# Performance work log

Measured on AMD Instinct MI355X. Metric: run time of the kernel, lower is better.

The kernel has to match this reference:

```python
import jax, jax.numpy as jnp
import numpy as np

# dims
B, A, L, P = 8, 64, 256, 20
T_HIST, SD, MF = 10, 8, 6
H, NH, NL = 256, 8, 3
C, S = 64, 30
# config scalars
DT, MAX_SPEED, MAX_ACCEL, MAX_CURV, SAFETY = 0.1, 15.0, 5.0, 0.3, 1.5
CW, BW, LAW = 1.0, 0.1, 0.5
MAX_STEP = MAX_SPEED * DT
LN_EPS = 1e-5


def _ln(x, g, b):
    m = x.mean(-1, keepdims=True)
    v = ((x - m) ** 2).mean(-1, keepdims=True)
    return (x - m) / jnp.sqrt(v + LN_EPS) * g + b


def setup_inputs() -> dict:
    key = jax.random.key(0)
    ks = jax.random.split(key, 24)
    f32 = jnp.float32
    def rn(k, shape, s=0.02):
        return jax.random.normal(k, shape, dtype=f32) * s
    return {
        'ego_history': jax.random.normal(ks[0], (B, T_HIST, SD), dtype=f32),
        'agent_states': jax.random.normal(ks[1], (B, A, SD), dtype=f32) * 5.0,
        'map_polylines': jax.random.normal(ks[2], (B, L, P, MF), dtype=f32) * 5.0,
        # encoder params (jax layout: x @ W, W is [in, out])
        'enc_ego_w': rn(ks[3], (SD, H)), 'enc_ego_b': jnp.zeros((H,), f32),
        'enc_agent_w': rn(ks[4], (SD, H)), 'enc_agent_b': jnp.zeros((H,), f32),
        'enc_map_w': rn(ks[5], (MF, H)), 'enc_map_b': jnp.zeros((H,), f32),
        'enc_ln_g': jnp.ones((H,), f32), 'enc_ln_b': jnp.zeros((H,), f32),
        # shared cross-attention (torch MHA layout: in_proj [3H,H])
        'attn_in_w': rn(ks[6], (3 * H, H)), 'attn_in_b': jnp.zeros((3 * H,), f32),
        'attn_out_w': rn(ks[7], (H, H)), 'attn_out_b': jnp.zeros((H,), f32),
        # per-layer MLPs, stacked over NL
        'mlp_w1': rn(ks[8], (NL, H, 2 * H)), 'mlp_b1': jnp.zeros((NL, 2 * H), f32),
        'mlp_w2': rn(ks[9], (NL, 2 * H, H)), 'mlp_b2': jnp.zeros((NL, H), f32),
        'pl_ln_g': jnp.ones((H,), f32), 'pl_ln_b': jnp.zeros((H,), f32),
        # heads
        'traj_w': rn(ks[10], (H, C * S * 2)), 'traj_b': jnp.zeros((C * S * 2,), f32),
        'score_w': rn(ks[11], (H, C)), 'score_b': jnp.zeros((C,), f32),
    }


def reference(ego_history, agent_states, map_polylines,
              enc_ego_w, enc_ego_b, enc_agent_w, enc_agent_b, enc_map_w, enc_map_b,
              enc_ln_g, enc_ln_b,
              attn_in_w, attn_in_b, attn_out_w, attn_out_b,
              mlp_w1, mlp_b1, mlp_w2, mlp_b2,
              pl_ln_g, pl_ln_b, traj_w, traj_b, score_w, score_b):
    # ---- vector encoder ----
    ego_tok = (ego_history[:, -1] @ enc_ego_w + enc_ego_b)[:, None, :]       # [B,1,H]
    agent_tok = agent_states @ enc_agent_w + enc_agent_b                     # [B,A,H]
    map_tok = (map_polylines @ enc_map_w + enc_map_b).mean(axis=2)           # [B,L,H]
    tokens = _ln(jnp.concatenate([ego_tok, agent_tok, map_tok], axis=1), enc_ln_g, enc_ln_b)
    lane_points = map_polylines[..., :2]                                     # [B,L,P,2]

    # ---- planner core: shared cross-attn, per-layer MLP, shared LayerNorm ----
    hd = H // NH
    wq, wk, wv = jnp.split(attn_in_w, 3, axis=0)
    bq, bk, bv = jnp.split(attn_in_b, 3)
    K = (tokens @ wk.T + bk).reshape(B, -1, NH, hd).transpose(0, 2, 1, 3)    # [B,h,N,d]
    V = (tokens @ wv.T + bv).reshape(B, -1, NH, hd).transpose(0, 2, 1, 3)
    fused = tokens[:, :1, :]                                                 # ego query [B,1,H]
    for i in range(NL):
        Q = (fused @ wq.T + bq).reshape(B, 1, NH, hd).transpose(0, 2, 1, 3)
        att = jax.nn.softmax(jnp.einsum('bhqd,bhkd->bhqk', Q, K) / (hd ** 0.5), axis=-1)
        attended = jnp.einsum('bhqk,bhkd->bhqd', att, V).transpose(0, 2, 1, 3).reshape(B, 1, H)
        attended = attended @ attn_out_w.T + attn_out_b
        h = jax.nn.gelu(fused @ mlp_w1[i] + mlp_b1[i], approximate=False)
        fused = _ln(fused + attended + (h @ mlp_w2[i] + mlp_b2[i]), pl_ln_g, pl_ln_b)
    fused = fused[:, 0, :]                                                   # [B,H]

    deltas = jnp.tanh((fused @ traj_w + traj_b).reshape(B, C, S, 2)) * MAX_STEP
    start_xy = ego_history[:, -1, :2]
    traj = start_xy[:, None, None, :] + jnp.cumsum(deltas, axis=2)           # [B,C,S,2]
    logits = fused @ score_w + score_b                                       # [B,C]
    scores = jax.nn.softmax(logits, axis=-1)

    # ---- kinematic feasibility ----
    vel = (traj[:, :, 1:] - traj[:, :, :-1]) / DT                            # [B,C,S-1,2]
    acc = (vel[:, :, 1:] - vel[:, :, :-1]) / DT
    d1 = traj[:, :, 1:] - traj[:, :, :-1]
    dd = d1[:, :, 1:] - d1[:, :, :-1]
    cross = d1[:, :, :-1, 0] * dd[..., 1] - d1[:, :, :-1, 1] * dd[..., 0]
    curv = jnp.abs(cross) / jnp.clip(jnp.linalg.norm(d1[:, :, :-1], axis=-1) ** 3, 1e-6)
    feasible = ((jnp.linalg.norm(vel, axis=-1).max(-1) <= MAX_SPEED)
                & (jnp.linalg.norm(acc, axis=-1).max(-1) <= MAX_ACCEL)
                & (curv.max(-1) <= MAX_CURV))                                # [B,C]

    # ---- collision check against agent positions ----
    cdiff = traj[:, :, :, None, :] - agent_states[:, None, None, :, :2]      # [B,C,S,A,2]
    min_distance = jnp.linalg.norm(cdiff, axis=-1).min(axis=(2, 3))          # [B,C]
    collision_free = min_distance >= SAFETY

    # ---- lane distance: pairwise min over (steps, lanes, points) ----
    t = traj.reshape(B, C * S, 2)
    lp = lane_points.reshape(B, L * P, 2)
    d2m = (jnp.sum(t * t, -1)[:, :, None] + jnp.sum(lp * lp, -1)[:, None, :]
           - 2.0 * jnp.einsum('bnx,bmx->bnm', t, lp))                        # [B,C*S,L*P]
    lane_distance = jnp.sqrt(jnp.clip(d2m, 0.0)).reshape(B, C, S * L * P).min(-1)
    lane_mask = lane_distance <= SAFETY * 3.0

    ldir = (lane_points[:, :, -1, :] - lane_points[:, :, 0, :]).mean(axis=1)
    ldir = ldir / jnp.clip(jnp.linalg.norm(ldir, axis=-1, keepdims=True), 1e-6)
    tdir = traj[:, :, -1, :] - traj[:, :, 0, :]
    tdir = tdir / jnp.clip(jnp.linalg.norm(tdir, axis=-1, keepdims=True), 1e-6)
    lane_alignment = jnp.sum(tdir * ldir[:, None, :], -1)                    # [B,C]

    # ---- masked selection ----
    valid = feasible & collision_free & lane_mask & (lane_alignment >= 0.0)
    safe_scores = jnp.where(valid, scores, -1.0)
    selected_index = jnp.where(valid.any(-1), safe_scores.argmax(-1), scores.argmax(-1))
    selected_trajectory = jnp.take_along_axis(traj, selected_index[:, None, None, None], axis=1)[:, 0]

    constraint_cost = (CW * jax.nn.relu(SAFETY - min_distance)
                       + BW * lane_distance + LAW * jax.nn.relu(1.0 - lane_alignment))
    return (traj, logits, scores, selected_index, selected_trajectory,
            min_distance, lane_distance, lane_alignment, constraint_cost)
```

## Files before the change

### kernel.cpp

```cpp
#include <hip/hip_runtime.h>
#include <math.h>
#include <stddef.h>

#define B_   8
#define A_   64
#define L_   256
#define P_   20
#define SD_  8
#define MF_  6
#define H_   256
#define NH_  8
#define HD_  32
#define NL_  3
#define C_   64
#define S_   30
#define N_   321
#define NTOK (B_*N_)

__device__ inline float waveSum(float v){
#pragma unroll
  for(int o=32;o;o>>=1) v += __shfl_down(v,o,64);
  return v;
}

__global__ void __launch_bounds__(256) k_prep_encode(
    const float* __restrict__ ego, const float* __restrict__ agents,
    const float* __restrict__ mp,
    const float* __restrict__ w_ego, const float* __restrict__ b_ego,
    const float* __restrict__ w_ag,  const float* __restrict__ b_ag,
    const float* __restrict__ w_map, const float* __restrict__ b_map,
    const float* __restrict__ ln_g,  const float* __restrict__ ln_b,
    const float* __restrict__ attn_in_w, const float* __restrict__ attn_out_w,
    float* __restrict__ tokens,
    float* __restrict__ wqT, float* __restrict__ wkT,
    float* __restrict__ wvT, float* __restrict__ aowT,
    float* __restrict__ ldir){
  int blk = blockIdx.x;
  int j = threadIdx.x;
  __shared__ float tile_s[64][65];
  __shared__ float in_s[SD_];
  __shared__ __align__(16) float arr[120];
  __shared__ float red[8];

  if(blk < NTOK){
    int b = blk / N_;
    int n = blk % N_;
    const float* W; const float* bias; int D;
    if(n==0){
      if(j<SD_) in_s[j] = ego[(b*10 + 9)*SD_ + j];
      W=w_ego; bias=b_ego; D=SD_;
    } else if(n<=A_){
      int a=n-1;
      if(j<SD_) in_s[j] = agents[(size_t)(b*A_+a)*SD_ + j];
      W=w_ag; bias=b_ag; D=SD_;
    } else {
      int l=n-1-A_;
      if(j<30) ((float4*)arr)[j] = ((const float4*)(mp + (size_t)(b*L_+l)*120))[j];
      __syncthreads();
      if(j<MF_){
        float s=0.f;
#pragma unroll
        for(int p=0;p<P_;p++) s += arr[p*MF_+j];
        in_s[j] = s * (1.0f/P_);
      }
      W=w_map; bias=b_map; D=MF_;
    }
    __syncthreads();
    float acc = bias[j];
    for(int d=0;d<D;d++) acc += in_s[d]*W[d*H_ + j];
    float s1=acc, s2=acc*acc;
#pragma unroll
    for(int o=32;o;o>>=1){ s1+=__shfl_down(s1,o,64); s2+=__shfl_down(s2,o,64); }
    if((j&63)==0){ red[j>>6]=s1; red[4+(j>>6)]=s2; }
    __syncthreads();
    float m = (red[0]+red[1]+red[2]+red[3]) * (1.0f/H_);
    float v = (red[4]+red[5]+red[6]+red[7]) * (1.0f/H_) - m*m;
    tokens[(size_t)blk*H_ + j] = (acc-m)*rsqrtf(v+1e-5f)*ln_g[j] + ln_b[j];
  } else if(blk < NTOK+64){
    int tid2 = blk - NTOK;
    int mat = tid2 >> 4;
    int tile = tid2 & 15;
    int jt = (tile>>2)*64, dt = (tile&3)*64;
    const float* src; float* dst;
    if(mat==0){ src = attn_in_w;            dst = wqT; }
    else if(mat==1){ src = attn_in_w + 256*H_; dst = wkT; }
    else if(mat==2){ src = attn_in_w + 512*H_; dst = wvT; }
    else { src = attn_out_w; dst = aowT; }
    int c = j & 63, r0 = (j>>6)*16;
#pragma unroll
    for(int r=0;r<16;r++) tile_s[r0+r][c] = src[(size_t)(jt + r0 + r)*H_ + dt + c];
    __syncthreads();
#pragma unroll
    for(int r=0;r<16;r++) dst[(size_t)(dt + r0 + r)*H_ + jt + c] = tile_s[c][r0+r];
  } else {
    int b = blk - (NTOK+64);
    const float* p0 = mp + (size_t)(b*L_ + j)*120;
    float dx = p0[19*MF_+0]-p0[0];
    float dy = p0[19*MF_+1]-p0[1];
#pragma unroll
    for(int o=32;o;o>>=1){ dx+=__shfl_down(dx,o,64); dy+=__shfl_down(dy,o,64); }
    if((j&63)==0){ red[j>>6]=dx; red[4+(j>>6)]=dy; }
    __syncthreads();
    if(j==0){
      float sx = (red[0]+red[1]+red[2]+red[3])*(1.0f/L_);
      float sy = (red[4]+red[5]+red[6]+red[7])*(1.0f/L_);
      float nm = fmaxf(sqrtf(sx*sx+sy*sy), 1e-6f);
      ldir[b*2]=sx/nm; ldir[b*2+1]=sy/nm;
    }
  }
}

__global__ void __launch_bounds__(256) k_kv(
    const float* __restrict__ tokens,
    const float* __restrict__ wkT, const float* __restrict__ wvT,
    const float* __restrict__ attn_in_b,
    float* __restrict__ K, float* __restrict__ V){
  int base = blockIdx.x * 8;
  int j = threadIdx.x;
  __shared__ float tok_s[8][H_];
#pragma unroll
  for(int t=0;t<8;t++) tok_s[t][j] = tokens[(size_t)(base+t)*H_ + j];
  __syncthreads();
  float bk = attn_in_b[256+j], bv = attn_in_b[512+j];
  float aK[8], aV[8];
#pragma unroll
  for(int t=0;t<8;t++){ aK[t]=bk; aV[t]=bv; }
#pragma unroll 4
  for(int d=0;d<H_;d++){
    float wk = wkT[d*H_+j], wv = wvT[d*H_+j];
#pragma unroll
    for(int t=0;t<8;t++){ float x=tok_s[t][d]; aK[t]+=x*wk; aV[t]+=x*wv; }
  }
#pragma unroll
  for(int t=0;t<8;t++){
    K[(size_t)(base+t)*H_+j]=aK[t];
    V[(size_t)(base+t)*H_+j]=aV[t];
  }
}

__global__ void __launch_bounds__(512) k_attn_mlp1(
    const float* __restrict__ tokens, const float* __restrict__ y_in,
    const float* __restrict__ K, const float* __restrict__ V,
    const float* __restrict__ wqT, const float* __restrict__ attn_in_b,
    const float* __restrict__ mlp_w1, const float* __restrict__ mlp_b1,
    const float* __restrict__ pl_g, const float* __restrict__ pl_b,
    float* __restrict__ fusedv, float* __restrict__ h1v,
    float* __restrict__ attv, int layer){
  const int b = blockIdx.x & 7, h = blockIdx.x >> 3;
  const int t = threadIdx.x;
  __shared__ __align__(16) float x_s[H_];
  __shared__ __align__(16) float q_s[HD_];
  __shared__ float att_s[N_+7];
  __shared__ float part1[512];
  __shared__ float part2[512];
  __shared__ float redA[8], redB[8];

  float yv = 0.f;
  if(t < H_){
    if(layer==0){
      x_s[t] = tokens[((size_t)b*N_)*H_ + t];
    } else {
      yv = y_in[b*H_ + t];
      float s1=yv, s2=yv*yv;
#pragma unroll
      for(int o=32;o;o>>=1){ s1+=__shfl_down(s1,o,64); s2+=__shfl_down(s2,o,64); }
      if((t&63)==0){ redA[t>>6]=s1; redB[t>>6]=s2; }
    }
  }
  __syncthreads();
  if(layer!=0 && t < H_){
    float m = (redA[0]+redA[1]+redA[2]+redA[3])*(1.0f/H_);
    float v = (redB[0]+redB[1]+redB[2]+redB[3])*(1.0f/H_) - m*m;
    x_s[t] = (yv-m)*rsqrtf(v+1e-5f)*pl_g[t] + pl_b[t];
  }
  __syncthreads();
  if(h==0 && t < H_) fusedv[b*H_+t] = x_s[t];

  {
    int c=t&31, ks=t>>5;
    const float* w = wqT + (size_t)(ks*16)*H_ + h*HD_ + c;
    float a=0.f;
#pragma unroll
    for(int d=0;d<16;d++) a += x_s[ks*16+d]*w[(size_t)d*H_];
    part1[t]=a;
  }
  {
    int c2=t&63, k2=t>>6;
    const float* w1 = mlp_w1 + (size_t)layer*H_*512 + (size_t)(k2*32)*512 + h*64 + c2;
    float a=0.f;
#pragma unroll
    for(int d=0;d<32;d++) a += x_s[k2*32+d]*w1[(size_t)d*512];
    part2[t]=a;
  }
  __syncthreads();
  if(t<32){
    float q = attn_in_b[h*HD_+t];
#pragma unroll
    for(int ks=0;ks<16;ks++) q += part1[ks*32+t];
    q_s[t]=q;
  }
  if(t<64){
    float v = mlp_b1[layer*512 + h*64 + t];
#pragma unroll
    for(int k2=0;k2<8;k2++) v += part2[k2*64+t];
    h1v[b*512 + h*64 + t] = v*0.5f*(1.0f+erff(v*0.70710678118654752f));
  }
  __syncthreads();

  float s0 = -3.0e38f;
  if(t < N_){
    const float4* kp=(const float4*)(K + ((size_t)(b*N_+t))*H_ + h*HD_);
    const float4* qp=(const float4*)q_s;
    float s=0.f;
#pragma unroll
    for(int i=0;i<8;i++){ float4 kk=kp[i], qq=qp[i]; s+=kk.x*qq.x+kk.y*qq.y+kk.z*qq.z+kk.w*qq.w; }
    s0 = s*0.17677669529663687f;
  }
  float mx = s0;
#pragma unroll
  for(int o=32;o;o>>=1) mx = fmaxf(mx, __shfl_xor(mx,o,64));
  if((t&63)==0) redA[t>>6]=mx;
  __syncthreads();
  mx = fmaxf(fmaxf(fmaxf(redA[0],redA[1]),fmaxf(redA[2],redA[3])),
             fmaxf(fmaxf(redA[4],redA[5]),fmaxf(redA[6],redA[7])));
  float p0 = 0.f;
  if(t < N_){ p0 = expf(s0-mx); att_s[t]=p0; }
  float lsum = p0;
#pragma unroll
  for(int o=32;o;o>>=1) lsum += __shfl_xor(lsum,o,64);
  if((t&63)==0) redB[t>>6]=lsum;
  __syncthreads();

  {
    int o=t&31, ks=t>>5;
    int n0=ks*20, n1=(ks==15)?N_:n0+20;
    const float* Vp = V + ((size_t)(b*N_))*H_ + h*HD_ + o;
    float a=0.f;
#pragma unroll 5
    for(int n=n0;n<n1;n++) a += att_s[n]*Vp[(size_t)n*H_];
    part1[t]=a;
  }
  __syncthreads();
  if(t<32){
    float inv = 1.0f/(redB[0]+redB[1]+redB[2]+redB[3]+redB[4]+redB[5]+redB[6]+redB[7]);
    float a=0.f;
#pragma unroll
    for(int ks=0;ks<16;ks++) a += part1[ks*32+t];
    attv[b*H_ + h*HD_ + t] = a*inv;
  }
}

__global__ void __launch_bounds__(512) k_out_mlp2(
    const float* __restrict__ attv, const float* __restrict__ h1v,
    const float* __restrict__ fusedv,
    const float* __restrict__ aowT, const float* __restrict__ attn_out_b,
    const float* __restrict__ mlp_w2, const float* __restrict__ mlp_b2,
    float* __restrict__ y, int layer){
  int b  = blockIdx.x >> 4;
  int cg = blockIdx.x & 15;
  int t = threadIdx.x;
  int c = t & 15, rs = t >> 4;
  int col = cg*16 + c;
  __shared__ float xa_s[H_];
  __shared__ float xh_s[512];
  __shared__ float part[16][33];
  if(t < H_) xa_s[t] = attv[b*H_ + t];
  xh_s[t] = h1v[b*512 + t];
  __syncthreads();
  float acc = 0.f;
  int r0 = rs*24, r1 = r0+24;
  int rEndA = r1 < 256 ? r1 : 256;
#pragma unroll 8
  for(int r=r0; r<rEndA; ++r) acc += xa_s[r]*aowT[(size_t)r*H_ + col];
  const float* w2 = mlp_w2 + (size_t)layer*512*H_;
  int rBegB = r0 > 256 ? r0 : 256;
#pragma unroll 8
  for(int r=rBegB; r<r1; ++r){
    int rr = r-256;
    acc += xh_s[rr]*w2[(size_t)rr*H_ + col];
  }
  part[c][rs] = acc;
  __syncthreads();
  if(t < 16){
    int colo = cg*16 + t;
    float s = 0.f;
#pragma unroll
    for(int k=0;k<32;k++) s += part[t][k];
    y[b*H_ + colo] = s + attn_out_b[colo] + mlp_b2[layer*H_ + colo] + fusedv[b*H_ + colo];
  }
}

__global__ void __launch_bounds__(256) k_decode_constraints(
    const float* __restrict__ y, const float* __restrict__ pl_g,
    const float* __restrict__ pl_b,
    const float* __restrict__ traj_w, const float* __restrict__ traj_b,
    const float* __restrict__ score_w, const float* __restrict__ score_b,
    const float* __restrict__ ego,
    const float* __restrict__ agents, const float* __restrict__ mp,
    const float* __restrict__ ldir,
    float* __restrict__ o_traj, float* __restrict__ o_logits,
    float* __restrict__ o_mind, float* __restrict__ o_laned,
    float* __restrict__ o_align, float* __restrict__ o_cost,
    float* __restrict__ valid){
  int b = blockIdx.x >> 6, c = blockIdx.x & 63;
  int t = threadIdx.x;
  int j = t & 63, sl = t >> 6;
  __shared__ float fs[H_];
  __shared__ float part[4][64];
  __shared__ float ds[60];
  __shared__ float ts[60];
  __shared__ float as_[A_*2];
  __shared__ float red[8];
  __shared__ float redsc[4];
  __shared__ int bad;
  float yv = y[b*H_ + t];
  float s1=yv, s2=yv*yv;
#pragma unroll
  for(int o=32;o;o>>=1){ s1+=__shfl_down(s1,o,64); s2+=__shfl_down(s2,o,64); }
  if((t&63)==0){ red[t>>6]=s1; red[4+(t>>6)]=s2; }
  if(t==0) bad=0;
  __syncthreads();
  {
    float m = (red[0]+red[1]+red[2]+red[3])*(1.0f/H_);
    float v = (red[4]+red[5]+red[6]+red[7])*(1.0f/H_) - m*m;
    fs[t] = (yv-m)*rsqrtf(v+1e-5f)*pl_g[t] + pl_b[t];
  }
  __syncthreads();
  if(j < 60){
    int col = c*60 + j;
    const float* w = traj_w + (size_t)(sl*64)*3840 + col;
    float acc=0.f;
#pragma unroll 16
    for(int d=0;d<64;d++) acc += fs[sl*64+d]*w[(size_t)d*3840];
    part[sl][j] = acc;
  }
  float lp = fs[t]*score_w[t*64 + c];
  lp = waveSum(lp);
  if((t&63)==0) redsc[t>>6]=lp;
  if(t>=128 && t<256){ int q=t-128; as_[q] = agents[(size_t)(b*A_ + (q>>1))*SD_ + (q&1)]; }
  __syncthreads();
  if(t < 60){
    float a = part[0][t]+part[1][t]+part[2][t]+part[3][t] + traj_b[c*60+t];
    ds[t] = tanhf(a)*1.5f;
  }
  if(t==0) o_logits[b*64+c] = redsc[0]+redsc[1]+redsc[2]+redsc[3] + score_b[c];
  __syncthreads();
  if(t<2){
    float x = ego[(b*10+9)*SD_ + t];
    for(int s=0;s<S_;s++){ x += ds[s*2+t]; ts[s*2+t] = x; }
  }
  __syncthreads();
  if(t<60) o_traj[(size_t)(b*64+c)*60 + t] = ts[t];
  if(t<29){
    float dx = ts[2*t+2]-ts[2*t], dy = ts[2*t+3]-ts[2*t+1];
    if((dx*dx+dy*dy)*100.0f > 225.0f) bad=1;
  }
  if(t<28){
    float x0=ts[2*t],y0=ts[2*t+1],x1=ts[2*t+2],y1=ts[2*t+3],x2=ts[2*t+4],y2=ts[2*t+5];
    float ddx = x2-2.f*x1+x0, ddy = y2-2.f*y1+y0;
    if((ddx*ddx+ddy*ddy)*10000.0f > 25.0f) bad=1;
    float d1x=x1-x0, d1y=y1-y0;
    float cross = d1x*ddy - d1y*ddx;
    float n2 = d1x*d1x+d1y*d1y;
    float n3 = fmaxf(n2*sqrtf(n2), 1e-6f);
    if(fabsf(cross) > 0.3f*n3) bad=1;
  }
  float md2 = 3.0e38f;
  for(int idx=t; idx<S_*A_; idx+=256){
    int s = idx>>6, a = idx&63;
    float dx = ts[2*s]-as_[2*a], dy = ts[2*s+1]-as_[2*a+1];
    md2 = fminf(md2, dx*dx+dy*dy);
  }
  float lx[20], ly[20];
#pragma unroll
  for(int k=0;k<20;k++){
    int i = t + k*256;
    const float* pp = mp + (size_t)(b*5120 + i)*MF_;
    lx[k]=pp[0]; ly[k]=pp[1];
  }
  float ld2 = 3.0e38f;
  for(int s=0;s<S_;s++){
    float tx=ts[2*s], ty=ts[2*s+1];
#pragma unroll
    for(int k=0;k<20;k++){
      float dx=tx-lx[k], dy=ty-ly[k];
      ld2 = fminf(ld2, dx*dx+dy*dy);
    }
  }
  __syncthreads();
#pragma unroll
  for(int o=32;o;o>>=1) md2 = fminf(md2, __shfl_down(md2,o,64));
  if((t&63)==0) red[t>>6]=md2;
  __syncthreads();
  md2 = fminf(fminf(red[0],red[1]),fminf(red[2],red[3]));
  __syncthreads();
#pragma unroll
  for(int o=32;o;o>>=1) ld2 = fminf(ld2, __shfl_down(ld2,o,64));
  if((t&63)==0) red[t>>6]=ld2;
  __syncthreads();
  ld2 = fminf(fminf(red[0],red[1]),fminf(red[2],red[3]));
  if(t==0){
    float md = sqrtf(md2), ld = sqrtf(ld2);
    float tdx = ts[58]-ts[0], tdy = ts[59]-ts[1];
    float nm = fmaxf(sqrtf(tdx*tdx+tdy*tdy), 1e-6f);
    tdx/=nm; tdy/=nm;
    float al = tdx*ldir[b*2] + tdy*ldir[b*2+1];
    int ok = (!bad) && (md>=1.5f) && (ld<=4.5f) && (al>=0.0f);
    int oi = b*64+c;
    o_mind[oi]=md; o_laned[oi]=ld; o_align[oi]=al;
    o_cost[oi] = fmaxf(1.5f-md,0.0f) + 0.1f*ld + 0.5f*fmaxf(1.0f-al,0.0f);
    valid[oi] = ok ? 1.0f : 0.0f;
  }
}

__global__ void __launch_bounds__(64) k_select(
    const float* __restrict__ logits, const float* __restrict__ valid,
    const float* __restrict__ o_traj,
    float* __restrict__ o_scores,
    float* __restrict__ o_selidx, float* __restrict__ o_seltraj){
  int b = blockIdx.x; int t = threadIdx.x;
  float lg = logits[b*64+t];
  float mx = lg;
#pragma unroll
  for(int o=32;o;o>>=1) mx = fmaxf(mx, __shfl_xor(mx,o,64));
  float e = expf(lg-mx);
  float sm = e;
#pragma unroll
  for(int o=32;o;o>>=1) sm += __shfl_xor(sm,o,64);
  float sc = e/sm;
  o_scores[b*64+t] = sc;
  bool v = valid[b*64+t] > 0.5f;
  unsigned long long bal = __ballot(v);
  float sv = v ? sc : -1.0f;
  float v1=sv; int i1=t;
  float v2=sc; int i2=t;
#pragma unroll
  for(int o=32;o;o>>=1){
    float ov=__shfl_down(v1,o,64); int oi=__shfl_down(i1,o,64);
    if(ov>v1 || (ov==v1 && oi<i1)){ v1=ov; i1=oi; }
    ov=__shfl_down(v2,o,64); oi=__shfl_down(i2,o,64);
    if(ov>v2 || (ov==v2 && oi<i2)){ v2=ov; i2=oi; }
  }
  int sel = (bal!=0ULL) ? i1 : i2;
  sel = __shfl(sel, 0, 64);
  if(t==0) o_selidx[b] = (float)sel;
  if(t<60) o_seltraj[b*60+t] = o_traj[(size_t)(b*64+sel)*60 + t];
}

extern "C" void kernel_launch(void* const* d_in, const int* in_sizes, int n_in,
                              void* d_out, int out_size, void* d_ws, size_t ws_size,
                              hipStream_t stream) {
  const float* ego        = (const float*)d_in[0];
  const float* agents     = (const float*)d_in[1];
  const float* mp         = (const float*)d_in[2];
  const float* enc_ego_w  = (const float*)d_in[3];
  const float* enc_ego_b  = (const float*)d_in[4];
  const float* enc_ag_w   = (const float*)d_in[5];
  const float* enc_ag_b   = (const float*)d_in[6];
  const float* enc_map_w  = (const float*)d_in[7];
  const float* enc_map_b  = (const float*)d_in[8];
  const float* enc_ln_g   = (const float*)d_in[9];
  const float* enc_ln_b   = (const float*)d_in[10];
  const float* attn_in_w  = (const float*)d_in[11];
  const float* attn_in_b  = (const float*)d_in[12];
  const float* attn_out_w = (const float*)d_in[13];
  const float* attn_out_b = (const float*)d_in[14];
  const float* mlp_w1     = (const float*)d_in[15];
  const float* mlp_b1     = (const float*)d_in[16];
  const float* mlp_w2     = (const float*)d_in[17];
  const float* mlp_b2     = (const float*)d_in[18];
  const float* pl_ln_g    = (const float*)d_in[19];
  const float* pl_ln_b    = (const float*)d_in[20];
  const float* traj_w     = (const float*)d_in[21];
  const float* traj_b     = (const float*)d_in[22];
  const float* score_w    = (const float*)d_in[23];
  const float* score_b    = (const float*)d_in[24];

  float* out = (float*)d_out;
  float* o_traj    = out;
  float* o_logits  = out + 30720;
  float* o_scores  = out + 31232;
  float* o_selidx  = out + 31744;
  float* o_seltraj = out + 31752;
  float* o_mind    = out + 32232;
  float* o_laned   = out + 32744;
  float* o_align   = out + 33256;
  float* o_cost    = out + 33768;

  float* ws = (float*)d_ws;
  float* tokens = ws;
  float* K      = ws + 657408;
  float* V      = ws + 1314816;
  float* wqT    = ws + 1972224;
  float* wkT    = ws + 2037760;
  float* wvT    = ws + 2103296;
  float* aowT   = ws + 2168832;
  float* fusedv = ws + 2234368;
  float* yv     = ws + 2236416;
  float* h1v    = ws + 2238464;
  float* attv   = ws + 2242560;
  float* ldir   = ws + 2244608;
  float* validv = ws + 2244624;

  k_prep_encode<<<NTOK+64+8,256,0,stream>>>(ego, agents, mp,
      enc_ego_w, enc_ego_b, enc_ag_w, enc_ag_b, enc_map_w, enc_map_b,
      enc_ln_g, enc_ln_b, attn_in_w, attn_out_w,
      tokens, wqT, wkT, wvT, aowT, ldir);
  k_kv<<<NTOK/8,256,0,stream>>>(tokens, wkT, wvT, attn_in_b, K, V);
  for(int i=0;i<NL_;i++){
    k_attn_mlp1<<<B_*NH_,512,0,stream>>>(tokens, yv, K, V, wqT, attn_in_b,
        mlp_w1, mlp_b1, pl_ln_g, pl_ln_b, fusedv, h1v, attv, i);
    k_out_mlp2<<<B_*16,512,0,stream>>>(attv, h1v, fusedv, aowT, attn_out_b,
        mlp_w2, mlp_b2, yv, i);
  }
  k_decode_constraints<<<B_*C_,256,0,stream>>>(yv, pl_ln_g, pl_ln_b,
      traj_w, traj_b, score_w, score_b, ego, agents, mp, ldir,
      o_traj, o_logits, o_mind, o_laned, o_align, o_cost, validv);
  k_select<<<B_,64,0,stream>>>(o_logits, validv, o_traj, o_scores, o_selidx, o_seltraj);
}
```

Before: 196.6 us.

## Fuse per-layer attention and MLP kernels into one persistent kernel with batch barriers

Replaces the six per-layer launches (attention+MLP1 and out-proj+MLP2 for each of three layers) with a single 64-block kernel. Loops over layers in-kernel and uses atomic-counter barriers across the 8 head blocks of each batch element instead of kernel boundaries. The out-projection/MLP2 work is redistributed so each head block computes 32 output columns. It also drops the fusedv buffer by reusing the block's own x_s. This removes launch overhead and inter-kernel gaps. In exchange it relies on all 64 blocks being co-resident for the spin barriers, and the barrier counters are reset by the previous kernel.

```diff
diff --git a/kernel.cpp b/kernel.cpp
--- a/kernel.cpp
+++ b/kernel.cpp
@@ -23,6 +23,17 @@
   return v;
 }
 
+__device__ inline void batchBarrier(unsigned* cnt){
+  __syncthreads();
+  if(threadIdx.x==0){
+    __threadfence();
+    atomicAdd(cnt, 1u);
+    while(atomicAdd(cnt, 0u) < 8u){}
+    __threadfence();
+  }
+  __syncthreads();
+}
+
 __global__ void __launch_bounds__(256) k_prep_encode(
     const float* __restrict__ ego, const float* __restrict__ agents,
     const float* __restrict__ mp,
@@ -34,13 +45,15 @@
     float* __restrict__ tokens,
     float* __restrict__ wqT, float* __restrict__ wkT,
     float* __restrict__ wvT, float* __restrict__ aowT,
-    float* __restrict__ ldir){
+    float* __restrict__ ldir, unsigned* __restrict__ bar){
   int blk = blockIdx.x;
   int j = threadIdx.x;
   __shared__ float tile_s[64][65];
   __shared__ float in_s[SD_];
   __shared__ __align__(16) float arr[120];
   __shared__ float red[8];
+
+  if(blk==0 && j<64) bar[j] = 0u;
 
   if(blk < NTOK){
     int b = blk / N_;
@@ -138,155 +151,150 @@
   }
 }
 
-__global__ void __launch_bounds__(512) k_attn_mlp1(
-    const float* __restrict__ tokens, const float* __restrict__ y_in,
+__global__ void __launch_bounds__(512) k_layers(
+    const float* __restrict__ tokens,
     const float* __restrict__ K, const float* __restrict__ V,
     const float* __restrict__ wqT, const float* __restrict__ attn_in_b,
     const float* __restrict__ mlp_w1, const float* __restrict__ mlp_b1,
+    const float* __restrict__ aowT, const float* __restrict__ attn_out_b,
+    const float* __restrict__ mlp_w2, const float* __restrict__ mlp_b2,
     const float* __restrict__ pl_g, const float* __restrict__ pl_b,
-    float* __restrict__ fusedv, float* __restrict__ h1v,
-    float* __restrict__ attv, int layer){
+    float* __restrict__ h1v, float* __restrict__ attv,
+    float* __restrict__ yv, unsigned* __restrict__ bar){
   const int b = blockIdx.x & 7, h = blockIdx.x >> 3;
   const int t = threadIdx.x;
   __shared__ __align__(16) float x_s[H_];
   __shared__ __align__(16) float q_s[HD_];
-  __shared__ float att_s[N_+7];
-  __shared__ float part1[512];
-  __shared__ float part2[512];
+  __shared__ __align__(16) float U[1360];
   __shared__ float redA[8], redB[8];
 
-  float yv = 0.f;
-  if(t < H_){
-    if(layer==0){
-      x_s[t] = tokens[((size_t)b*N_)*H_ + t];
-    } else {
-      yv = y_in[b*H_ + t];
-      float s1=yv, s2=yv*yv;
-#pragma unroll
-      for(int o=32;o;o>>=1){ s1+=__shfl_down(s1,o,64); s2+=__shfl_down(s2,o,64); }
-      if((t&63)==0){ redA[t>>6]=s1; redB[t>>6]=s2; }
-    }
-  }
-  __syncthreads();
-  if(layer!=0 && t < H_){
-    float m = (redA[0]+redA[1]+redA[2]+redA[3])*(1.0f/H_);
-    float v = (redB[0]+redB[1]+redB[2]+redB[3])*(1.0f/H_) - m*m;
-    x_s[t] = (yv-m)*rsqrtf(v+1e-5f)*pl_g[t] + pl_b[t];
-  }
-  __syncthreads();
-  if(h==0 && t < H_) fusedv[b*H_+t] = x_s[t];
-
-  {
-    int c=t&31, ks=t>>5;
-    const float* w = wqT + (size_t)(ks*16)*H_ + h*HD_ + c;
-    float a=0.f;
-#pragma unroll
-    for(int d=0;d<16;d++) a += x_s[ks*16+d]*w[(size_t)d*H_];
-    part1[t]=a;
-  }
-  {
-    int c2=t&63, k2=t>>6;
-    const float* w1 = mlp_w1 + (size_t)layer*H_*512 + (size_t)(k2*32)*512 + h*64 + c2;
-    float a=0.f;
-#pragma unroll
-    for(int d=0;d<32;d++) a += x_s[k2*32+d]*w1[(size_t)d*512];
-    part2[t]=a;
-  }
-  __syncthreads();
-  if(t<32){
-    float q = attn_in_b[h*HD_+t];
-#pragma unroll
-    for(int ks=0;ks<16;ks++) q += part1[ks*32+t];
-    q_s[t]=q;
-  }
-  if(t<64){
-    float v = mlp_b1[layer*512 + h*64 + t];
-#pragma unroll
-    for(int k2=0;k2<8;k2++) v += part2[k2*64+t];
-    h1v[b*512 + h*64 + t] = v*0.5f*(1.0f+erff(v*0.70710678118654752f));
-  }
-  __syncthreads();
-
-  float s0 = -3.0e38f;
-  if(t < N_){
-    const float4* kp=(const float4*)(K + ((size_t)(b*N_+t))*H_ + h*HD_);
-    const float4* qp=(const float4*)q_s;
-    float s=0.f;
-#pragma unroll
-    for(int i=0;i<8;i++){ float4 kk=kp[i], qq=qp[i]; s+=kk.x*qq.x+kk.y*qq.y+kk.z*qq.z+kk.w*qq.w; }
-    s0 = s*0.17677669529663687f;
-  }
-  float mx = s0;
-#pragma unroll
-  for(int o=32;o;o>>=1) mx = fmaxf(mx, __shfl_xor(mx,o,64));
-  if((t&63)==0) redA[t>>6]=mx;
-  __syncthreads();
-  mx = fmaxf(fmaxf(fmaxf(redA[0],redA[1]),fmaxf(redA[2],redA[3])),
-             fmaxf(fmaxf(redA[4],redA[5]),fmaxf(redA[6],redA[7])));
-  float p0 = 0.f;
-  if(t < N_){ p0 = expf(s0-mx); att_s[t]=p0; }
-  float lsum = p0;
-#pragma unroll
-  for(int o=32;o;o>>=1) lsum += __shfl_xor(lsum,o,64);
-  if((t&63)==0) redB[t>>6]=lsum;
-  __syncthreads();
-
-  {
-    int o=t&31, ks=t>>5;
-    int n0=ks*20, n1=(ks==15)?N_:n0+20;
-    const float* Vp = V + ((size_t)(b*N_))*H_ + h*HD_ + o;
-    float a=0.f;
+  for(int layer=0; layer<NL_; ++layer){
+    float* att_s = U;
+    float* part1 = U + 336;
+    float* part2 = U + 848;
+    float yvv = 0.f;
+    if(t < H_){
+      if(layer==0){
+        x_s[t] = tokens[((size_t)b*N_)*H_ + t];
+      } else {
+        yvv = yv[b*H_ + t];
+        float s1=yvv, s2=yvv*yvv;
+#pragma unroll
+        for(int o=32;o;o>>=1){ s1+=__shfl_down(s1,o,64); s2+=__shfl_down(s2,o,64); }
+        if((t&63)==0){ redA[t>>6]=s1; redB[t>>6]=s2; }
+      }
+    }
+    __syncthreads();
+    if(layer!=0 && t < H_){
+      float m = (redA[0]+redA[1]+redA[2]+redA[3])*(1.0f/H_);
+      float v = (redB[0]+redB[1]+redB[2]+redB[3])*(1.0f/H_) - m*m;
+      x_s[t] = (yvv-m)*rsqrtf(v+1e-5f)*pl_g[t] + pl_b[t];
+    }
+    __syncthreads();
+
+    {
+      int c=t&31, ks=t>>5;
+      const float* w = wqT + (size_t)(ks*16)*H_ + h*HD_ + c;
+      float a=0.f;
+#pragma unroll
+      for(int d=0;d<16;d++) a += x_s[ks*16+d]*w[(size_t)d*H_];
+      part1[t]=a;
+    }
+    {
+      int c2=t&63, k2=t>>6;
+      const float* w1 = mlp_w1 + (size_t)layer*H_*512 + (size_t)(k2*32)*512 + h*64 + c2;
+      float a=0.f;
+#pragma unroll
+      for(int d=0;d<32;d++) a += x_s[k2*32+d]*w1[(size_t)d*512];
+      part2[t]=a;
+    }
+    __syncthreads();
+    if(t<32){
+      float q = attn_in_b[h*HD_+t];
+#pragma unroll
+      for(int ks=0;ks<16;ks++) q += part1[ks*32+t];
+      q_s[t]=q;
+    }
+    if(t<64){
+      float v = mlp_b1[layer*512 + h*64 + t];
+#pragma unroll
+      for(int k2=0;k2<8;k2++) v += part2[k2*64+t];
+      h1v[b*512 + h*64 + t] = v*0.5f*(1.0f+erff(v*0.70710678118654752f));
+    }
+    __syncthreads();
+
+    float s0 = -3.0e38f;
+    if(t < N_){
+      const float4* kp=(const float4*)(K + ((size_t)(b*N_+t))*H_ + h*HD_);
+      const float4* qp=(const float4*)q_s;
+      float s=0.f;
+#pragma unroll
+      for(int i=0;i<8;i++){ float4 kk=kp[i], qq=qp[i]; s+=kk.x*qq.x+kk.y*qq.y+kk.z*qq.z+kk.w*qq.w; }
+      s0 = s*0.17677669529663687f;
+    }
+    float mx = s0;
+#pragma unroll
+    for(int o=32;o;o>>=1) mx = fmaxf(mx, __shfl_xor(mx,o,64));
+    if((t&63)==0) redA[t>>6]=mx;
+    __syncthreads();
+    mx = fmaxf(fmaxf(fmaxf(redA[0],redA[1]),fmaxf(redA[2],redA[3])),
+               fmaxf(fmaxf(redA[4],redA[5]),fmaxf(redA[6],redA[7])));
+    float p0 = 0.f;
+    if(t < N_){ p0 = expf(s0-mx); att_s[t]=p0; }
+    float lsum = p0;
+#pragma unroll
+    for(int o=32;o;o>>=1) lsum += __shfl_xor(lsum,o,64);
+    if((t&63)==0) redB[t>>6]=lsum;
+    __syncthreads();
+
+    {
+      int o=t&31, ks=t>>5;
+      int n0=ks*20, n1=(ks==15)?N_:n0+20;
+      const float* Vp = V + ((size_t)(b*N_))*H_ + h*HD_ + o;
+      float a=0.f;
 #pragma unroll 5
-    for(int n=n0;n<n1;n++) a += att_s[n]*Vp[(size_t)n*H_];
-    part1[t]=a;
-  }
-  __syncthreads();
-  if(t<32){
-    float inv = 1.0f/(redB[0]+redB[1]+redB[2]+redB[3]+redB[4]+redB[5]+redB[6]+redB[7]);
-    float a=0.f;
-#pragma unroll
-    for(int ks=0;ks<16;ks++) a += part1[ks*32+t];
-    attv[b*H_ + h*HD_ + t] = a*inv;
-  }
-}
-
-__global__ void __launch_bounds__(512) k_out_mlp2(
-    const float* __restrict__ attv, const float* __restrict__ h1v,
-    const float* __restrict__ fusedv,
-    const float* __restrict__ aowT, const float* __restrict__ attn_out_b,
-    const float* __restrict__ mlp_w2, const float* __restrict__ mlp_b2,
-    float* __restrict__ y, int layer){
-  int b  = blockIdx.x >> 4;
-  int cg = blockIdx.x & 15;
-  int t = threadIdx.x;
-  int c = t & 15, rs = t >> 4;
-  int col = cg*16 + c;
-  __shared__ float xa_s[H_];
-  __shared__ float xh_s[512];
-  __shared__ float part[16][33];
-  if(t < H_) xa_s[t] = attv[b*H_ + t];
-  xh_s[t] = h1v[b*512 + t];
-  __syncthreads();
-  float acc = 0.f;
-  int r0 = rs*24, r1 = r0+24;
-  int rEndA = r1 < 256 ? r1 : 256;
+      for(int n=n0;n<n1;n++) a += att_s[n]*Vp[(size_t)n*H_];
+      part1[t]=a;
+    }
+    __syncthreads();
+    if(t<32){
+      float inv = 1.0f/(redB[0]+redB[1]+redB[2]+redB[3]+redB[4]+redB[5]+redB[6]+redB[7]);
+      float a=0.f;
+#pragma unroll
+      for(int ks=0;ks<16;ks++) a += part1[ks*32+t];
+      attv[b*H_ + h*HD_ + t] = a*inv;
+    }
+    batchBarrier(bar + layer*16 + b);
+
+    float* xa_s  = U;
+    float* xh_s  = U + 256;
+    float* partB = U + 768;
+    xh_s[t] = h1v[b*512 + t];
+    if(t < H_) xa_s[t] = attv[b*H_ + t];
+    __syncthreads();
+    {
+      int c=t&31, rs=t>>5;
+      int col = h*32 + c;
+      float a=0.f;
+      int r0=rs*48, r1=r0+48;
+      int rEndA = r1 < 256 ? r1 : 256;
 #pragma unroll 8
-  for(int r=r0; r<rEndA; ++r) acc += xa_s[r]*aowT[(size_t)r*H_ + col];
-  const float* w2 = mlp_w2 + (size_t)layer*512*H_;
-  int rBegB = r0 > 256 ? r0 : 256;
+      for(int r=r0; r<rEndA; ++r) a += xa_s[r]*aowT[(size_t)r*H_ + col];
+      const float* w2 = mlp_w2 + (size_t)layer*512*H_;
+      int rBegB = r0 > 256 ? r0 : 256;
 #pragma unroll 8
-  for(int r=rBegB; r<r1; ++r){
-    int rr = r-256;
-    acc += xh_s[rr]*w2[(size_t)rr*H_ + col];
-  }
-  part[c][rs] = acc;
-  __syncthreads();
-  if(t < 16){
-    int colo = cg*16 + t;
-    float s = 0.f;
-#pragma unroll
-    for(int k=0;k<32;k++) s += part[t][k];
-    y[b*H_ + colo] = s + attn_out_b[colo] + mlp_b2[layer*H_ + colo] + fusedv[b*H_ + colo];
+      for(int r=rBegB; r<r1; ++r){ int rr=r-256; a += xh_s[rr]*w2[(size_t)rr*H_ + col]; }
+      partB[c*17+rs]=a;
+    }
+    __syncthreads();
+    if(t<32){
+      float s=0.f;
+#pragma unroll
+      for(int k=0;k<16;k++) s += partB[t*17+k];
+      int colo = h*32+t;
+      yv[b*H_+colo] = s + attn_out_b[colo] + mlp_b2[layer*H_+colo] + x_s[colo];
+    }
+    if(layer != NL_-1) batchBarrier(bar + layer*16 + 8 + b);
   }
 }
 
@@ -495,24 +503,21 @@
   float* wkT    = ws + 2037760;
   float* wvT    = ws + 2103296;
   float* aowT   = ws + 2168832;
-  float* fusedv = ws + 2234368;
   float* yv     = ws + 2236416;
   float* h1v    = ws + 2238464;
   float* attv   = ws + 2242560;
   float* ldir   = ws + 2244608;
   float* validv = ws + 2244624;
+  unsigned* bar = (unsigned*)(ws + 2245136);
 
   k_prep_encode<<<NTOK+64+8,256,0,stream>>>(ego, agents, mp,
       enc_ego_w, enc_ego_b, enc_ag_w, enc_ag_b, enc_map_w, enc_map_b,
       enc_ln_g, enc_ln_b, attn_in_w, attn_out_w,
-      tokens, wqT, wkT, wvT, aowT, ldir);
+      tokens, wqT, wkT, wvT, aowT, ldir, bar);
   k_kv<<<NTOK/8,256,0,stream>>>(tokens, wkT, wvT, attn_in_b, K, V);
-  for(int i=0;i<NL_;i++){
-    k_attn_mlp1<<<B_*NH_,512,0,stream>>>(tokens, yv, K, V, wqT, attn_in_b,
-        mlp_w1, mlp_b1, pl_ln_g, pl_ln_b, fusedv, h1v, attv, i);
-    k_out_mlp2<<<B_*16,512,0,stream>>>(attv, h1v, fusedv, aowT, attn_out_b,
-        mlp_w2, mlp_b2, yv, i);
-  }
+  k_layers<<<B_*NH_,512,0,stream>>>(tokens, K, V, wqT, attn_in_b,
+      mlp_w1, mlp_b1, aowT, attn_out_b, mlp_w2, mlp_b2,
+      pl_ln_g, pl_ln_b, h1v, attv, yv, bar);
   k_decode_constraints<<<B_*C_,256,0,stream>>>(yv, pl_ln_g, pl_ln_b,
       traj_w, traj_b, score_w, score_b, ego, agents, mp, ldir,
       o_traj, o_logits, o_mind, o_laned, o_align, o_cost, validv);
```

After: 220.3 us. +12.0%, slower.
